# Kernel tuning notes

Measured on AMD Instinct MI355X. Metric: run time of the kernel, lower is better.

## Reference

```python
import jax, jax.numpy as jnp
import numpy as np
import math

HEAD = 16
D_MODEL = 1024
HEAD_DIM = D_MODEL // HEAD
B, S = 2, 2048


def setup_inputs() -> dict:
    key = jax.random.key(0)
    ks = jax.random.split(key, 9)
    sc = 1.0 / math.sqrt(D_MODEL)
    return {
        "q": jax.random.normal(ks[0], (B, S, D_MODEL), dtype=jnp.float32),
        "k": jax.random.normal(ks[1], (B, S, D_MODEL), dtype=jnp.float32),
        "v": jax.random.normal(ks[2], (B, S, D_MODEL), dtype=jnp.float32),
        "mask": jax.random.randint(ks[3], (B, 1, S, S), 0, 2, dtype=jnp.int32),
        "wq": jax.random.normal(ks[4], (D_MODEL, D_MODEL), dtype=jnp.float32) * sc,
        "wk": jax.random.normal(ks[5], (D_MODEL, D_MODEL), dtype=jnp.float32) * sc,
        "wv": jax.random.normal(ks[6], (D_MODEL, D_MODEL), dtype=jnp.float32) * sc,
        "wo": jax.random.normal(ks[7], (D_MODEL, D_MODEL), dtype=jnp.float32) * sc,
        "bo": jax.random.normal(ks[8], (D_MODEL,), dtype=jnp.float32) * 0.01,
    }


def reference(q, k, v, mask, wq, wk, wv, wo, bo):
    N, Lq, _ = q.shape
    Lk = k.shape[1]
    # projections (bias-free linears)
    qh = (q @ wq).reshape(N, Lq, HEAD, HEAD_DIM)
    kh = (k @ wk).reshape(N, Lk, HEAD, HEAD_DIM)
    vh = (v @ wv).reshape(N, Lk, HEAD, HEAD_DIM)
    # full [N, H, Lq, Lk] score matrix, as in original
    scores = jnp.einsum('nqha,nkha->nhqk', qh, kh)
    scores = jnp.where(mask == 0, jnp.float32(-1e10), scores)
    attn = jax.nn.softmax(scores / math.sqrt(HEAD_DIM), axis=-1)
    out = jnp.einsum('nhqk,nkha->nqha', attn, vh).reshape(N, Lq, D_MODEL)
    return out @ wo + bo
```

## Files before the change

kernel.cpp:

```cpp
#include <hip/hip_runtime.h>

typedef unsigned short ushort_t;
typedef __attribute__((ext_vector_type(8))) __bf16 bf16x8;
typedef __attribute__((ext_vector_type(4))) float f32x4;
typedef __attribute__((ext_vector_type(4))) unsigned int u32x4;
typedef __attribute__((ext_vector_type(4))) unsigned short u16x4;

#define NB 2
#define SS 2048
#define NH 16
#define DH 64
#define DM 1024
#define MM 4096

#define QK_SCALE 0.1803368801111204f

__device__ __forceinline__ ushort_t f2bf(float f){
  unsigned u = __builtin_bit_cast(unsigned, f);
  unsigned r = u + 0x7FFFu + ((u >> 16) & 1u);
  return (ushort_t)(r >> 16);
}

__device__ __forceinline__ void load_lds16(const void* g, void* l){
  __builtin_amdgcn_global_load_lds(
      (const __attribute__((address_space(1))) unsigned int*)g,
      (__attribute__((address_space(3))) unsigned int*)l, 16, 0, 0);
}

__global__ __launch_bounds__(256) void cvt3(const float* __restrict__ q,
                                            const float* __restrict__ k,
                                            const float* __restrict__ v,
                                            ushort_t* qo, ushort_t* ko, ushort_t* vo, int n){
  int z = blockIdx.z;
  const float* src = (z == 0) ? q : (z == 1) ? k : v;
  ushort_t* dst    = (z == 0) ? qo : (z == 1) ? ko : vo;
  int i = (blockIdx.x * blockDim.x + threadIdx.x) * 4;
  if (i < n){
    f32x4 w = *(const f32x4*)(src + i);
    u16x4 o = { f2bf(w[0]), f2bf(w[1]), f2bf(w[2]), f2bf(w[3]) };
    *(u16x4*)(dst + i) = o;
  }
}

__global__ __launch_bounds__(256) void wtrans4(const float* __restrict__ W0, const float* __restrict__ W1,
                                               const float* __restrict__ W2, const float* __restrict__ W3,
                                               ushort_t* T0, ushort_t* T1, ushort_t* T2, ushort_t* T3){
  __shared__ float t[32][33];
  int z = blockIdx.z;
  const float* W = (z == 0) ? W0 : (z == 1) ? W1 : (z == 2) ? W2 : W3;
  ushort_t* Wt   = (z == 0) ? T0 : (z == 1) ? T1 : (z == 2) ? T2 : T3;
  int k0 = blockIdx.x * 32, n0 = blockIdx.y * 32;
  int tx = threadIdx.x, ty = threadIdx.y;
  #pragma unroll
  for (int i = 0; i < 4; i++)
    t[ty + 8*i][tx] = W[(size_t)(k0 + ty + 8*i) * DM + (n0 + tx)];
  __syncthreads();
  #pragma unroll
  for (int i = 0; i < 4; i++)
    Wt[(size_t)(n0 + ty + 8*i) * DM + (k0 + tx)] = f2bf(t[tx][ty + 8*i]);
}

__global__ __launch_bounds__(256) void mask_expand(const int* __restrict__ mask,
                                                   ushort_t* __restrict__ mexp){
  int id = blockIdx.x * 4 + (threadIdx.x >> 6);
  int lane = threadIdx.x & 63;
  int t = id & 31; int q = (id >> 5) & (SS - 1); int b = id >> 16;
  int m = mask[((size_t)b * SS + q) * SS + t * 64 + lane];
  unsigned long long bits = __ballot(m != 0);
  int g = lane >> 4, rem = lane & 15;
  int c = rem >> 3, i = (rem >> 1) & 3, h = rem & 1;
  int kv = (2*c + (i >> 1)) * 16 + 4*g + 2*(i & 1) + h;
  ushort_t out = (ushort_t)(((bits >> kv) & 1ULL) ? 0xFFFFu : 0u);
  mexp[(((size_t)b * SS + q) * 32 + t) * 64 + lane] = out;
}

__global__ __launch_bounds__(256) void vtrans(const ushort_t* __restrict__ vh,
                                              ushort_t* __restrict__ vt){
  __shared__ ushort_t t[64][65];
  int bh = blockIdx.y, s0 = blockIdx.x * 64;
  int tid = threadIdx.x;
  const ushort_t* src = vh + (size_t)bh * SS * DH + (size_t)s0 * DH;
  #pragma unroll
  for (int i = 0; i < 2; i++){
    int id = tid + 256*i; int r = id >> 3, c = id & 7;
    union { u32x4 v; ushort_t s[8]; } u;
    u.v = *(const u32x4*)(src + r*64 + c*8);
    #pragma unroll
    for (int j = 0; j < 8; j++) t[r][c*8 + j] = u.s[j];
  }
  __syncthreads();
  ushort_t* dst = vt + (size_t)bh * DH * SS;
  #pragma unroll
  for (int i = 0; i < 2; i++){
    int id = tid + 256*i; int d = id >> 3, c8 = id & 7;
    union { u32x4 v; ushort_t s[8]; } u;
    #pragma unroll
    for (int j = 0; j < 8; j++){
      int p = c8*8 + j;
      int srck = ((p >> 5) << 5) + (((p & 7) >> 2) << 4) + (((p >> 3) & 3) << 2) + (p & 3);
      u.s[j] = t[srck][d];
    }
    *(u32x4*)(dst + (size_t)d * SS + s0 + c8*8) = u.v;
  }
}

__global__ __launch_bounds__(256) void gemm_qkv(
    const ushort_t* A0, const ushort_t* A1, const ushort_t* A2,
    const ushort_t* B0, const ushort_t* B1, const ushort_t* B2,
    ushort_t* C0, ushort_t* C1, ushort_t* C2){
  __shared__ __align__(16) char smem[32768];
  char* As = smem; char* Bs = smem + 16384;
  int z = blockIdx.z;
  const ushort_t* A  = (z == 0) ? A0 : (z == 1) ? A1 : A2;
  const ushort_t* Bt = (z == 0) ? B0 : (z == 1) ? B1 : B2;
  ushort_t* Cb       = (z == 0) ? C0 : (z == 1) ? C1 : C2;

  int m0 = blockIdx.x * 128, n0 = blockIdx.y * 128;
  int tid = threadIdx.x, wid = tid >> 6, lane = tid & 63;
  int lc = lane & 15, g = lane >> 4;
  int wm = wid >> 1, wn = wid & 1;

  f32x4 acc[4][4] = {};
  for (int kt = 0; kt < DM / 64; kt++){
    __syncthreads();
    int k0 = kt * 64;
    #pragma unroll
    for (int i = 0; i < 4; i++){
      int id = tid + 256*i; int r = id >> 3, c = id & 7;
      load_lds16(A  + (size_t)(m0 + r) * DM + k0 + ((c ^ (r & 7)) << 3), As + id*16);
      load_lds16(Bt + (size_t)(n0 + r) * DM + k0 + ((c ^ (r & 7)) << 3), Bs + id*16);
    }
    __syncthreads();
    #pragma unroll
    for (int f = 0; f < 2; f++){
      bf16x8 af[4], bfr[4];
      #pragma unroll
      for (int i = 0; i < 4; i++){
        int ar = wm*64 + i*16 + lc;
        af[i] = *(const bf16x8*)(As + ar*128 + (((f*4 + g) ^ (ar & 7)) << 4));
        int br = wn*64 + i*16 + lc;
        bfr[i] = *(const bf16x8*)(Bs + br*128 + (((f*4 + g) ^ (br & 7)) << 4));
      }
      #pragma unroll
      for (int mi = 0; mi < 4; mi++)
        #pragma unroll
        for (int ni = 0; ni < 4; ni++)
          acc[mi][ni] = __builtin_amdgcn_mfma_f32_16x16x32_bf16(af[mi], bfr[ni], acc[mi][ni], 0, 0, 0);
    }
  }
  float oscale = (z == 0) ? QK_SCALE : 1.0f;
  #pragma unroll
  for (int mi = 0; mi < 4; mi++)
    #pragma unroll
    for (int ni = 0; ni < 4; ni++)
      #pragma unroll
      for (int reg = 0; reg < 4; reg++){
        int m = m0 + wm*64 + mi*16 + g*4 + reg;
        int n = n0 + wn*64 + ni*16 + lc;
        int b = m >> 11, s = m & (SS - 1), h = n >> 6, d = n & 63;
        Cb[(((size_t)(b*NH + h)) * SS + s) * DH + d] = f2bf(acc[mi][ni][reg] * oscale);
      }
}

__global__ __launch_bounds__(256) void gemm_wo(const ushort_t* __restrict__ A,
                                               const ushort_t* __restrict__ Bt,
                                               float* __restrict__ Cf,
                                               const float* __restrict__ bias){
  __shared__ __align__(16) char smem[24576];
  char* As = smem; char* Bs = smem + 16384;
  int m0 = blockIdx.x * 128, n0 = blockIdx.y * 64;
  int tid = threadIdx.x, wid = tid >> 6, lane = tid & 63;
  int lc = lane & 15, g = lane >> 4;
  int wm = wid >> 1, wn = wid & 1;

  f32x4 acc[4][2] = {};
  for (int kt = 0; kt < DM / 64; kt++){
    __syncthreads();
    int k0 = kt * 64;
    #pragma unroll
    for (int i = 0; i < 4; i++){
      int id = tid + 256*i; int r = id >> 3, c = id & 7;
      load_lds16(A + (size_t)(m0 + r) * DM + k0 + ((c ^ (r & 7)) << 3), As + id*16);
    }
    #pragma unroll
    for (int i = 0; i < 2; i++){
      int id = tid + 256*i; int r = id >> 3, c = id & 7;
      load_lds16(Bt + (size_t)(n0 + r) * DM + k0 + ((c ^ (r & 7)) << 3), Bs + id*16);
    }
    __syncthreads();
    #pragma unroll
    for (int f = 0; f < 2; f++){
      bf16x8 af[4], bfr[2];
      #pragma unroll
      for (int i = 0; i < 4; i++){
        int ar = wm*64 + i*16 + lc;
        af[i] = *(const bf16x8*)(As + ar*128 + (((f*4 + g) ^ (ar & 7)) << 4));
      }
      #pragma unroll
      for (int i = 0; i < 2; i++){
        int br = wn*32 + i*16 + lc;
        bfr[i] = *(const bf16x8*)(Bs + br*128 + (((f*4 + g) ^ (br & 7)) << 4));
      }
      #pragma unroll
      for (int mi = 0; mi < 4; mi++)
        #pragma unroll
        for (int ni = 0; ni < 2; ni++)
          acc[mi][ni] = __builtin_amdgcn_mfma_f32_16x16x32_bf16(af[mi], bfr[ni], acc[mi][ni], 0, 0, 0);
    }
  }
  #pragma unroll
  for (int mi = 0; mi < 4; mi++)
    #pragma unroll
    for (int ni = 0; ni < 2; ni++)
      #pragma unroll
      for (int reg = 0; reg < 4; reg++){
        int m = m0 + wm*64 + mi*16 + g*4 + reg;
        int n = n0 + wn*32 + ni*16 + lc;
        Cf[(size_t)m * DM + n] = acc[mi][ni][reg] + bias[n];
      }
}

__global__ __launch_bounds__(512, 4) void attn_fwd(
    const ushort_t* __restrict__ qh, const ushort_t* __restrict__ kh,
    const ushort_t* __restrict__ vt, const ushort_t* __restrict__ mexp,
    ushort_t* __restrict__ ao){
  __shared__ __align__(16) char smem[65536];

  int L = blockIdx.x + (SS/64) * blockIdx.y;
  int xcd = L & 7, slot = L >> 3;
  int bh = xcd * 4 + (slot >> 5);
  int q0 = (slot & 31) * 64;
  int b = bh >> 4;

  int tid = threadIdx.x, wid = tid >> 6, lane = tid & 63;
  int lc = lane & 15, g = lane >> 4;
  int half = wid >> 2, w4 = wid & 3;

  const size_t hoff = (size_t)bh * SS * DH;
  const ushort_t* Qb = qh + hoff;
  const ushort_t* Kb = kh + hoff;
  const ushort_t* Vb = vt + hoff;

  int qrow = q0 + w4*16 + lc;
  bf16x8 qf[2];
  #pragma unroll
  for (int c = 0; c < 2; c++)
    qf[c] = *(const bf16x8*)(Qb + (size_t)qrow * DH + c*32 + 8*g);

  const ushort_t* mb_lane = mexp + (((size_t)b * SS + qrow) * 32 + half*16) * 64 + g*16;

  int sw0 = ((0*4 + g) ^ (lc & 7)) << 4;
  int sw1 = ((1*4 + g) ^ (lc & 7)) << 4;

  bf16x8 onesf;
  { union { bf16x8 v; unsigned w[4]; } u;
    unsigned x = (lc == 0) ? 0x3F803F80u : 0u;
    u.w[0] = x; u.w[1] = x; u.w[2] = x; u.w[3] = x; onesf = u.v; }

  f32x4 o[4] = {};
  f32x4 o4 = {};

  auto stage = [&](int bufsel, int it){
    int kv0 = it * 64;
    char* dst = smem + bufsel * 32768;
    #pragma unroll
    for (int i = 0; i < 4; i++){
      int id = tid + 512*i;
      int tl = id >> 9; int r = (id >> 3) & 63; int c = id & 7;
      int hf = tl >> 1;
      const ushort_t* src = (tl & 1)
        ? Vb + (size_t)r * SS + hf*1024 + kv0 + ((c ^ (r & 7)) << 3)
        : Kb + (size_t)(hf*1024 + kv0 + r) * DH + ((c ^ (r & 7)) << 3);
      load_lds16(src, dst + id*16);
    }
  };

  stage(0, 0);
  __syncthreads();

  for (int it = 0; it < 16; it++){
    int cur = it & 1;
    if (it < 15) stage(cur ^ 1, it + 1);

    const char* Ks = smem + cur*32768 + half*16384;
    const char* Vs = Ks + 8192;

    u32x4 mwa = *(const u32x4*)(mb_lane + it*64);
    u32x4 mwb = *(const u32x4*)(mb_lane + it*64 + 8);

    f32x4 sc4[4];
    #pragma unroll
    for (int nt = 0; nt < 4; nt++){
      f32x4 a = {};
      const char* krow = Ks + (nt*16 + lc) * 128;
      bf16x8 kf0 = *(const bf16x8*)(krow + sw0);
      bf16x8 kf1 = *(const bf16x8*)(krow + sw1);
      a = __builtin_amdgcn_mfma_f32_16x16x32_bf16(kf0, qf[0], a, 0, 0, 0);
      a = __builtin_amdgcn_mfma_f32_16x16x32_bf16(kf1, qf[1], a, 0, 0, 0);
      sc4[nt] = a;
    }

    bf16x8 pa[2];
    #pragma unroll
    for (int c = 0; c < 2; c++){
      union { bf16x8 v; unsigned w[4]; } up;
      #pragma unroll
      for (int i = 0; i < 4; i++){
        int j0 = 2*i, j1 = 2*i + 1;
        float e0 = __builtin_amdgcn_exp2f(sc4[c*2 + (j0 >> 2)][j0 & 3]);
        float e1 = __builtin_amdgcn_exp2f(sc4[c*2 + (j1 >> 2)][j1 & 3]);
        unsigned lo = __builtin_bit_cast(unsigned, e0) + 0x8000u;
        unsigned hi = __builtin_bit_cast(unsigned, e1) + 0x8000u;
        up.w[i] = __builtin_amdgcn_perm(hi, lo, 0x07060302u) & (c ? mwb[i] : mwa[i]);
      }
      pa[c] = up.v;
    }

    #pragma unroll
    for (int c = 0; c < 2; c++){
      int off = c ? sw1 : sw0;
      #pragma unroll
      for (int dt = 0; dt < 4; dt++){
        bf16x8 vf = *(const bf16x8*)(Vs + (dt*16 + lc) * 128 + off);
        o[dt] = __builtin_amdgcn_mfma_f32_16x16x32_bf16(pa[c], vf, o[dt], 0, 0, 0);
      }
      o4 = __builtin_amdgcn_mfma_f32_16x16x32_bf16(pa[c], onesf, o4, 0, 0, 0);
    }

    __syncthreads();
  }

  float* Mo = (float*)smem;
  if (half == 1){
    #pragma unroll
    for (int reg = 0; reg < 4; reg++){
      int ql = w4*16 + g*4 + reg;
      #pragma unroll
      for (int dt = 0; dt < 4; dt++)
        Mo[ql*65 + dt*16 + lc] = o[dt][reg];
      if (lc == 0) Mo[ql*65 + 64] = o4[reg];
    }
  }
  __syncthreads();
  if (half == 0){
    #pragma unroll
    for (int reg = 0; reg < 4; reg++){
      int ql = w4*16 + g*4 + reg;
      float l0 = __shfl(o4[reg], lane & 48);
      float l1 = Mo[ql*65 + 64];
      float inv = 1.0f / (l0 + l1);
      int srow = q0 + ql;
      size_t base = ((size_t)b * SS + srow) * DM + (size_t)(bh & 15) * DH;
      #pragma unroll
      for (int dt = 0; dt < 4; dt++)
        ao[base + dt*16 + lc] = f2bf((o[dt][reg] + Mo[ql*65 + dt*16 + lc]) * inv);
    }
  }
}

extern "C" void kernel_launch(void* const* d_in, const int* in_sizes, int n_in,
                              void* d_out, int out_size, void* d_ws, size_t ws_size,
                              hipStream_t stream){
  const float* q    = (const float*)d_in[0];
  const float* k    = (const float*)d_in[1];
  const float* v    = (const float*)d_in[2];
  const int*   mask = (const int*)d_in[3];
  const float* wq   = (const float*)d_in[4];
  const float* wk   = (const float*)d_in[5];
  const float* wv   = (const float*)d_in[6];
  const float* wo   = (const float*)d_in[7];
  const float* bo   = (const float*)d_in[8];
  float* out = (float*)d_out;

  char* ws = (char*)d_ws;
  ushort_t* qb  = (ushort_t*)(ws + 0x0000000);
  ushort_t* kb  = (ushort_t*)(ws + 0x0800000);
  ushort_t* vb  = (ushort_t*)(ws + 0x1000000);
  ushort_t* wt0 = (ushort_t*)(ws + 0x1800000);
  ushort_t* wt1 = (ushort_t*)(ws + 0x1A00000);
  ushort_t* wt2 = (ushort_t*)(ws + 0x1C00000);
  ushort_t* wt3 = (ushort_t*)(ws + 0x1E00000);
  ushort_t* mexp = (ushort_t*)(ws + 0x2000000);
  ushort_t* qhB = (ushort_t*)(ws + 0x3000000);
  ushort_t* khB = (ushort_t*)(ws + 0x3800000);
  ushort_t* vhB = (ushort_t*)(ws + 0x4000000);
  ushort_t* vtB = (ushort_t*)(ws + 0x0000000);
  ushort_t* aoB = (ushort_t*)(ws + 0x4000000);

  const int nElem = MM * DM;
  cvt3<<<dim3(nElem/1024, 1, 3), 256, 0, stream>>>(q, k, v, qb, kb, vb, nElem);

  wtrans4<<<dim3(32, 32, 4), dim3(32, 8), 0, stream>>>(wq, wk, wv, wo, wt0, wt1, wt2, wt3);

  mask_expand<<<NB * SS * (SS/64) / 4, 256, 0, stream>>>(mask, mexp);

  gemm_qkv<<<dim3(MM/128, DM/128, 3), 256, 0, stream>>>(
      qb, kb, vb, wt0, wt1, wt2, qhB, khB, vhB);

  vtrans<<<dim3(SS/64, NB*NH), 256, 0, stream>>>(vhB, vtB);

  attn_fwd<<<dim3(SS/64, NB*NH), 512, 0, stream>>>(qhB, khB, vtB, mexp, aoB);

  gemm_wo<<<dim3(MM/128, DM/64), 256, 0, stream>>>(aoB, wt3, out, bo);
}
```

Baseline: 273.4 us.

## Restructure attention to 128-row query blocks and re-layout mask expansion

The attention kernel now has each of its 8 waves own 16 query rows of a 128-row block and iterate over the full KV length. This replaces the old scheme where two half-groups split the KV range and merged partial results through LDS. The mask expansion kernel now packs per-wave 16-row tiles into contiguous 1KB chunks, and attention prefetches the next tile's mask words one iteration ahead. Both GEMMs remap block indices so consecutive blocks spread across XCDs for better L2 locality. The trade-off is half as many attention blocks with twice the serial KV loop per block, but less LDS use and no final reduction step.

```diff
diff --git a/kernel.cpp b/kernel.cpp
--- a/kernel.cpp
+++ b/kernel.cpp
@@ -64,14 +64,30 @@
                                                    ushort_t* __restrict__ mexp){
   int id = blockIdx.x * 4 + (threadIdx.x >> 6);
   int lane = threadIdx.x & 63;
-  int t = id & 31; int q = (id >> 5) & (SS - 1); int b = id >> 16;
-  int m = mask[((size_t)b * SS + q) * SS + t * 64 + lane];
-  unsigned long long bits = __ballot(m != 0);
-  int g = lane >> 4, rem = lane & 15;
-  int c = rem >> 3, i = (rem >> 1) & 3, h = rem & 1;
-  int kv = (2*c + (i >> 1)) * 16 + 4*g + 2*(i & 1) + h;
-  ushort_t out = (ushort_t)(((bits >> kv) & 1ULL) ? 0xFFFFu : 0u);
-  mexp[(((size_t)b * SS + q) * 32 + t) * 64 + lane] = out;
+  int t = id & 31; int qgrp = (id >> 5) & 127; int b = id >> 12;
+  int lc = lane & 15, g = lane >> 4;
+
+  const int* mrow = mask + (((size_t)b * SS) + qgrp * 16) * SS + t * 64 + lane;
+  unsigned long long mybits = 0;
+  #pragma unroll
+  for (int r = 0; r < 16; r++){
+    unsigned long long bits = __ballot(mrow[(size_t)r * SS] != 0);
+    if (lc == r) mybits = bits;
+  }
+
+  unsigned w8[8];
+  #pragma unroll
+  for (int w = 0; w < 8; w++){
+    int c = w >> 2, i = w & 3;
+    int kv0 = (2*c + (i >> 1))*16 + 4*g + 2*(i & 1);
+    w8[w] = (((mybits >> kv0) & 1ULL) ? 0xFFFFu : 0u)
+          | (((mybits >> (kv0 + 1)) & 1ULL) ? 0xFFFF0000u : 0u);
+  }
+  ushort_t* dst = mexp + ((size_t)id) * 1024 + lane * 16;
+  u32x4 a = { w8[0], w8[1], w8[2], w8[3] };
+  u32x4 bb = { w8[4], w8[5], w8[6], w8[7] };
+  *(u32x4*)dst = a;
+  *(u32x4*)(dst + 8) = bb;
 }
 
 __global__ __launch_bounds__(256) void vtrans(const ushort_t* __restrict__ vh,
@@ -110,12 +126,16 @@
     ushort_t* C0, ushort_t* C1, ushort_t* C2){
   __shared__ __align__(16) char smem[32768];
   char* As = smem; char* Bs = smem + 16384;
-  int z = blockIdx.z;
+
+  int flat = blockIdx.x + 32 * blockIdx.y + 256 * blockIdx.z;
+  int nswz = (flat & 7) * 96 + (flat >> 3);
+  int z = nswz >> 8; int rem = nswz & 255;
+  int m0 = (rem & 31) * 128, n0 = (rem >> 5) * 128;
+
   const ushort_t* A  = (z == 0) ? A0 : (z == 1) ? A1 : A2;
   const ushort_t* Bt = (z == 0) ? B0 : (z == 1) ? B1 : B2;
   ushort_t* Cb       = (z == 0) ? C0 : (z == 1) ? C1 : C2;
 
-  int m0 = blockIdx.x * 128, n0 = blockIdx.y * 128;
   int tid = threadIdx.x, wid = tid >> 6, lane = tid & 63;
   int lc = lane & 15, g = lane >> 4;
   int wm = wid >> 1, wn = wid & 1;
@@ -168,7 +188,11 @@
                                                const float* __restrict__ bias){
   __shared__ __align__(16) char smem[24576];
   char* As = smem; char* Bs = smem + 16384;
-  int m0 = blockIdx.x * 128, n0 = blockIdx.y * 64;
+
+  int flat = blockIdx.x + 32 * blockIdx.y;
+  int nswz = (flat & 7) * 64 + (flat >> 3);
+  int m0 = (nswz & 31) * 128, n0 = (nswz >> 5) * 64;
+
   int tid = threadIdx.x, wid = tid >> 6, lane = tid & 63;
   int lc = lane & 15, g = lane >> 4;
   int wm = wid >> 1, wn = wid & 1;
@@ -224,30 +248,29 @@
     const ushort_t* __restrict__ qh, const ushort_t* __restrict__ kh,
     const ushort_t* __restrict__ vt, const ushort_t* __restrict__ mexp,
     ushort_t* __restrict__ ao){
-  __shared__ __align__(16) char smem[65536];
-
-  int L = blockIdx.x + (SS/64) * blockIdx.y;
+  __shared__ __align__(16) char smem[32768];
+
+  int L = blockIdx.x;
   int xcd = L & 7, slot = L >> 3;
-  int bh = xcd * 4 + (slot >> 5);
-  int q0 = (slot & 31) * 64;
+  int bh = xcd * 4 + (slot >> 4);
+  int q0 = (slot & 15) * 128;
   int b = bh >> 4;
 
   int tid = threadIdx.x, wid = tid >> 6, lane = tid & 63;
   int lc = lane & 15, g = lane >> 4;
-  int half = wid >> 2, w4 = wid & 3;
 
   const size_t hoff = (size_t)bh * SS * DH;
   const ushort_t* Qb = qh + hoff;
   const ushort_t* Kb = kh + hoff;
   const ushort_t* Vb = vt + hoff;
 
-  int qrow = q0 + w4*16 + lc;
+  int qrow = q0 + wid*16 + lc;
   bf16x8 qf[2];
   #pragma unroll
   for (int c = 0; c < 2; c++)
     qf[c] = *(const bf16x8*)(Qb + (size_t)qrow * DH + c*32 + 8*g);
 
-  const ushort_t* mb_lane = mexp + (((size_t)b * SS + qrow) * 32 + half*16) * 64 + g*16;
+  const ushort_t* mbase = mexp + (((size_t)b * 128 + (q0 >> 4) + wid) * 32) * 1024 + lane * 16;
 
   int sw0 = ((0*4 + g) ^ (lc & 7)) << 4;
   int sw1 = ((1*4 + g) ^ (lc & 7)) << 4;
@@ -262,31 +285,33 @@
 
   auto stage = [&](int bufsel, int it){
     int kv0 = it * 64;
-    char* dst = smem + bufsel * 32768;
-    #pragma unroll
-    for (int i = 0; i < 4; i++){
+    char* dst = smem + bufsel * 16384;
+    #pragma unroll
+    for (int i = 0; i < 2; i++){
       int id = tid + 512*i;
       int tl = id >> 9; int r = (id >> 3) & 63; int c = id & 7;
-      int hf = tl >> 1;
-      const ushort_t* src = (tl & 1)
-        ? Vb + (size_t)r * SS + hf*1024 + kv0 + ((c ^ (r & 7)) << 3)
-        : Kb + (size_t)(hf*1024 + kv0 + r) * DH + ((c ^ (r & 7)) << 3);
+      const ushort_t* src = tl
+        ? Vb + (size_t)r * SS + kv0 + ((c ^ (r & 7)) << 3)
+        : Kb + (size_t)(kv0 + r) * DH + ((c ^ (r & 7)) << 3);
       load_lds16(src, dst + id*16);
     }
   };
 
+  u32x4 mwa = *(const u32x4*)(mbase);
+  u32x4 mwb = *(const u32x4*)(mbase + 8);
   stage(0, 0);
   __syncthreads();
 
-  for (int it = 0; it < 16; it++){
+  for (int it = 0; it < 32; it++){
     int cur = it & 1;
-    if (it < 15) stage(cur ^ 1, it + 1);
-
-    const char* Ks = smem + cur*32768 + half*16384;
+    if (it < 31) stage(cur ^ 1, it + 1);
+
+    int itn = (it < 31) ? it + 1 : 31;
+    u32x4 mna = *(const u32x4*)(mbase + (size_t)itn * 1024);
+    u32x4 mnb = *(const u32x4*)(mbase + (size_t)itn * 1024 + 8);
+
+    const char* Ks = smem + cur*16384;
     const char* Vs = Ks + 8192;
-
-    u32x4 mwa = *(const u32x4*)(mb_lane + it*64);
-    u32x4 mwb = *(const u32x4*)(mb_lane + it*64 + 8);
 
     f32x4 sc4[4];
     #pragma unroll
@@ -328,33 +353,18 @@
     }
 
     __syncthreads();
-  }
-
-  float* Mo = (float*)smem;
-  if (half == 1){
-    #pragma unroll
-    for (int reg = 0; reg < 4; reg++){
-      int ql = w4*16 + g*4 + reg;
-      #pragma unroll
-      for (int dt = 0; dt < 4; dt++)
-        Mo[ql*65 + dt*16 + lc] = o[dt][reg];
-      if (lc == 0) Mo[ql*65 + 64] = o4[reg];
-    }
-  }
-  __syncthreads();
-  if (half == 0){
-    #pragma unroll
-    for (int reg = 0; reg < 4; reg++){
-      int ql = w4*16 + g*4 + reg;
-      float l0 = __shfl(o4[reg], lane & 48);
-      float l1 = Mo[ql*65 + 64];
-      float inv = 1.0f / (l0 + l1);
-      int srow = q0 + ql;
-      size_t base = ((size_t)b * SS + srow) * DM + (size_t)(bh & 15) * DH;
-      #pragma unroll
-      for (int dt = 0; dt < 4; dt++)
-        ao[base + dt*16 + lc] = f2bf((o[dt][reg] + Mo[ql*65 + dt*16 + lc]) * inv);
-    }
+    mwa = mna; mwb = mnb;
+  }
+
+  #pragma unroll
+  for (int reg = 0; reg < 4; reg++){
+    float l = __shfl(o4[reg], lane & 48);
+    float inv = 1.0f / l;
+    int srow = q0 + wid*16 + g*4 + reg;
+    size_t base = ((size_t)b * SS + srow) * DM + (size_t)(bh & 15) * DH;
+    #pragma unroll
+    for (int dt = 0; dt < 4; dt++)
+      ao[base + dt*16 + lc] = f2bf(o[dt][reg] * inv);
   }
 }
 
@@ -392,14 +402,14 @@
 
   wtrans4<<<dim3(32, 32, 4), dim3(32, 8), 0, stream>>>(wq, wk, wv, wo, wt0, wt1, wt2, wt3);
 
-  mask_expand<<<NB * SS * (SS/64) / 4, 256, 0, stream>>>(mask, mexp);
-
-  gemm_qkv<<<dim3(MM/128, DM/128, 3), 256, 0, stream>>>(
+  mask_expand<<<NB * 128 * 32 / 4, 256, 0, stream>>>(mask, mexp);
+
+  gemm_qkv<<<dim3(32, 8, 3), 256, 0, stream>>>(
       qb, kb, vb, wt0, wt1, wt2, qhB, khB, vhB);
 
   vtrans<<<dim3(SS/64, NB*NH), 256, 0, stream>>>(vhB, vtB);
 
-  attn_fwd<<<dim3(SS/64, NB*NH), 512, 0, stream>>>(qhB, khB, vtB, mexp, aoB);
-
-  gemm_wo<<<dim3(MM/128, DM/64), 256, 0, stream>>>(aoB, wt3, out, bo);
-}
+  attn_fwd<<<512, 512, 0, stream>>>(qhB, khB, vtB, mexp, aoB);
+
+  gemm_wo<<<dim3(32, 16), 256, 0, stream>>>(aoB, wt3, out, bo);
+}
```

New measurement: 262.8 us. -3.9%, faster.
